# Optimization experiments

Measured on AMD Instinct MI355X. Metric: run time of the kernel, lower is better.

Reference implementation:

```python
import jax, jax.numpy as jnp
import numpy as np

N_NODES = 50000
N_EDGES = 1600000
IN_CH = 128
HEADS = 4
OUT_PER_HEAD = 32  # out_channels // heads with concat=True
NEG_SLOPE = 0.2    # GATConv default leaky_relu slope
SOFTMAX_EPS = 1e-16  # PyG scatter-softmax denominator eps
LN_EPS = 1e-5


def setup_inputs() -> dict:
    key = jax.random.key(0)
    ks = jax.random.split(key, 8)
    x = jax.random.normal(ks[0], (N_NODES, IN_CH), dtype=jnp.float32)
    edge_index = jax.random.randint(ks[1], (2, N_EDGES), 0, N_NODES, dtype=jnp.int32)
    W = jax.random.normal(ks[2], (IN_CH, HEADS * OUT_PER_HEAD), dtype=jnp.float32) * (1.0 / np.sqrt(IN_CH))
    att_src = jax.random.normal(ks[3], (HEADS, OUT_PER_HEAD), dtype=jnp.float32) * 0.1
    att_dst = jax.random.normal(ks[4], (HEADS, OUT_PER_HEAD), dtype=jnp.float32) * 0.1
    bias = jnp.zeros((HEADS * OUT_PER_HEAD,), dtype=jnp.float32)
    gamma = jnp.ones((HEADS * OUT_PER_HEAD,), dtype=jnp.float32)
    beta = jnp.zeros((HEADS * OUT_PER_HEAD,), dtype=jnp.float32)
    return {"x": x, "edge_index": edge_index, "W": W, "att_src": att_src,
            "att_dst": att_dst, "bias": bias, "gamma": gamma, "beta": beta}


def reference(x, edge_index, W, att_src, att_dst, bias, gamma, beta):
    N = x.shape[0]
    H, C = att_src.shape
    # GATConv default add_self_loops=True
    loop = jnp.arange(N, dtype=edge_index.dtype)
    src = jnp.concatenate([edge_index[0], loop])  # message source j
    dst = jnp.concatenate([edge_index[1], loop])  # aggregation target i

    h = (x @ W).reshape(N, H, C)                      # [N,H,C]
    a_s = jnp.einsum('nhc,hc->nh', h, att_src)        # [N,H]
    a_d = jnp.einsum('nhc,hc->nh', h, att_dst)        # [N,H]

    logits = jax.nn.leaky_relu(a_s[src] + a_d[dst], NEG_SLOPE)  # [E,H]
    # segment softmax over edges grouped by destination node
    m = jax.ops.segment_max(logits, dst, num_segments=N)        # [N,H]
    m = jnp.where(jnp.isfinite(m), m, 0.0)
    e = jnp.exp(logits - m[dst])
    s = jax.ops.segment_sum(e, dst, num_segments=N)             # [N,H]
    alpha = e / (s[dst] + SOFTMAX_EPS)                          # [E,H]

    msg = h[src] * alpha[:, :, None]                            # [E,H,C]
    out = jax.ops.segment_sum(msg, dst, num_segments=N)         # [N,H,C]
    out = out.reshape(N, H * C) + bias

    mu = out.mean(axis=-1, keepdims=True)
    var = ((out - mu) ** 2).mean(axis=-1, keepdims=True)
    y = (out - mu) / jnp.sqrt(var + LN_EPS) * gamma + beta
    return jax.nn.elu(y)
```

## Files before the change

### kernel.cpp

```cpp
#include <hip/hip_runtime.h>
#include <hip/hip_bf16.h>

typedef __hip_bfloat16 bf16;
typedef unsigned int u32;
typedef unsigned short u16;

constexpr int N   = 50000;
constexpr int E   = 1600000;
constexpr int C   = 128;
constexpr int H   = 4;
constexpr int NB  = 782;
constexpr int CAP = 2560;
constexpr int CHUNK = 4096;
constexpr float NEG  = 0.2f;
constexpr float SEPS = 1e-16f;
constexpr float LEPS = 1e-5f;

__device__ __forceinline__ float lo16(u32 v) { return __uint_as_float(v << 16); }
__device__ __forceinline__ float hi16(u32 v) { return __uint_as_float(v & 0xFFFF0000u); }

__global__ __launch_bounds__(256) void k1_gemm(
    const float* __restrict__ x, const float* __restrict__ W,
    const float* __restrict__ att_s, const float* __restrict__ att_d,
    bf16* __restrict__ hb, float* __restrict__ as_, float* __restrict__ ad_)
{
    const int nb = blockIdx.x * 16;
    const int t  = threadIdx.x;
    __shared__ float sx[16 * 128];
    const float4* xg = (const float4*)(x + nb * 128);
    ((float4*)sx)[t]       = xg[t];
    ((float4*)sx)[t + 256] = xg[t + 256];
    __syncthreads();

    const int c = t & 127;
    const int g = t >> 7;
    const float* xb = sx + (g << 10);
    float acc[8] = {0.f, 0.f, 0.f, 0.f, 0.f, 0.f, 0.f, 0.f};

    for (int k = 0; k < 128; k += 4) {
        const float w0 = W[(k + 0) * 128 + c];
        const float w1 = W[(k + 1) * 128 + c];
        const float w2 = W[(k + 2) * 128 + c];
        const float w3 = W[(k + 3) * 128 + c];
#pragma unroll
        for (int j = 0; j < 8; ++j) {
            const float4 xv = *(const float4*)(xb + j * 128 + k);
            acc[j] = fmaf(xv.x, w0, fmaf(xv.y, w1, fmaf(xv.z, w2, fmaf(xv.w, w3, acc[j]))));
        }
    }

    const int lane = t & 63;
    const int head = c >> 5;
    const float asc = att_s[c], adc = att_d[c];
#pragma unroll
    for (int j = 0; j < 8; ++j) {
        const int node = nb + (g << 3) + j;
        hb[node * 128 + c] = __float2bfloat16(acc[j]);
        float vs = acc[j] * asc;
        float vd = acc[j] * adc;
#pragma unroll
        for (int off = 16; off; off >>= 1) {
            vs += __shfl_xor(vs, off, 64);
            vd += __shfl_xor(vd, off, 64);
        }
        if ((lane & 31) == 0) {
            as_[node * H + head] = vs;
            ad_[node * H + head] = vd;
        }
    }
}

__global__ __launch_bounds__(256) void kbin(
    const int* __restrict__ ei, u32* __restrict__ gcur, u32* __restrict__ pairs)
{
    __shared__ u32 lcnt[NB], lbase[NB], lfill[NB];
    const int t = threadIdx.x;
    const int base = blockIdx.x * CHUNK;
    const int nE = min(CHUNK, E - base);
    for (int i = t; i < NB; i += 256) lcnt[i] = 0;
    __syncthreads();
    for (int i = t; i < nE; i += 256)
        atomicAdd(&lcnt[((u32)ei[E + base + i]) >> 6], 1u);
    __syncthreads();
    for (int i = t; i < NB; i += 256) {
        u32 cb = lcnt[i];
        lbase[i] = cb ? atomicAdd(&gcur[i], cb) : 0u;
        lfill[i] = 0u;
    }
    __syncthreads();
    for (int i = t; i < nE; i += 256) {
        u32 src = (u32)ei[base + i];
        u32 dst = (u32)ei[E + base + i];
        u32 b = dst >> 6;
        u32 pos = atomicAdd(&lfill[b], 1u);
        pairs[(size_t)b * CAP + lbase[b] + pos] = src | ((dst & 63u) << 16);
    }
}

__global__ __launch_bounds__(64) void kscan(
    const u32* __restrict__ gcur, u32* __restrict__ bbase, int* __restrict__ row_ptr)
{
    const int t = threadIdx.x;
    u32 vals[13];
    u32 s = 0;
#pragma unroll
    for (int i = 0; i < 13; ++i) {
        int idx = t * 13 + i;
        u32 v = (idx < NB) ? gcur[idx] : 0u;
        vals[i] = s; s += v;
    }
    u32 incl = s;
#pragma unroll
    for (int off = 1; off < 64; off <<= 1) {
        u32 u = __shfl_up(incl, off, 64);
        if (t >= off) incl += u;
    }
    const u32 excl = incl - s;
#pragma unroll
    for (int i = 0; i < 13; ++i) {
        int idx = t * 13 + i;
        if (idx < NB) bbase[idx] = excl + vals[i];
    }
    if (t == 0) row_ptr[N] = E;
}

__global__ __launch_bounds__(256) void kfill2(
    const u32* __restrict__ pairs, const u32* __restrict__ gcur,
    const u32* __restrict__ bbase, int* __restrict__ row_ptr, u16* __restrict__ col)
{
    __shared__ int jcnt[64], joff[64], jcur[64];
    const int b = blockIdx.x, t = threadIdx.x;
    const int cntb = (int)gcur[b];
    const int base = (int)bbase[b];
    if (t < 64) jcnt[t] = 0;
    __syncthreads();
    const u32* pr = pairs + (size_t)b * CAP;
    for (int i = t; i < cntb; i += 256) atomicAdd(&jcnt[pr[i] >> 16], 1);
    __syncthreads();
    if (t < 64) {
        int v = jcnt[t], incl = v;
#pragma unroll
        for (int off = 1; off < 64; off <<= 1) {
            int u = __shfl_up(incl, off, 64);
            if (t >= off) incl += u;
        }
        joff[t] = incl - v;
        const int n = b * 64 + t;
        if (n < N) row_ptr[n] = base + joff[t];
        jcur[t] = 0;
    }
    __syncthreads();
    for (int i = t; i < cntb; i += 256) {
        const u32 p = pr[i];
        const int j = p >> 16;
        const int pos = atomicAdd(&jcur[j], 1);
        col[base + joff[j] + pos] = (u16)(p & 0xFFFFu);
    }
}

__global__ __launch_bounds__(256) void kd_agg_ln(
    const int* __restrict__ row_ptr, const u16* __restrict__ col,
    const u32* __restrict__ hb, const float* __restrict__ as_,
    const float* __restrict__ ad_,
    const float* __restrict__ bias, const float* __restrict__ gamma,
    const float* __restrict__ beta, float* __restrict__ out)
{
    __shared__ float wlds[4][64];
    const int tid  = threadIdx.x;
    const int lane = tid & 63;
    const int wv   = __builtin_amdgcn_readfirstlane(tid >> 6);
    const int n    = __builtin_amdgcn_readfirstlane((int)blockIdx.x * 4 + (tid >> 6));
    if (n >= N) return;

    const int head  = lane >> 4;
    const int eoff  = lane & 15;
    const int wbase = head << 4;
    float* __restrict__ wrow = wlds[wv];

    const float adn = ad_[n * H + head];
    const float asn = as_[n * H + head];

    float ls = asn + adn;
    ls = fmaxf(ls, NEG * ls);
    const float wself = __expf(ls);
    float den = (eoff == 0) ? wself : 0.f;
    const u32 hvs = hb[n * 64 + lane];
    float num0 = wself * lo16(hvs);
    float num1 = wself * hi16(hvs);

    const int k0  = row_ptr[n];
    const int end = row_ptr[n + 1];

    for (int k = k0; k < end; k += 16) {
        const int cnt = min(16, end - k);
        int   colv = 0;
        float w    = 0.f;
        if (eoff < cnt) {
            colv = col[k + eoff];
            const float a = as_[colv * H + head];
            float le = a + adn;
            le = fmaxf(le, NEG * le);
            w = __expf(le);
        }
        den += w;
        wrow[lane] = w;

        int e = 0;
        for (; e + 4 <= cnt; e += 4) {
            const float4 w4 = *(const float4*)(wrow + wbase + e);
            const int s0 = __builtin_amdgcn_readlane(colv, e + 0);
            const int s1 = __builtin_amdgcn_readlane(colv, e + 1);
            const int s2 = __builtin_amdgcn_readlane(colv, e + 2);
            const int s3 = __builtin_amdgcn_readlane(colv, e + 3);
            const u32 v0 = hb[s0 * 64 + lane];
            const u32 v1 = hb[s1 * 64 + lane];
            const u32 v2 = hb[s2 * 64 + lane];
            const u32 v3 = hb[s3 * 64 + lane];
            num0 = fmaf(w4.x, lo16(v0), num0); num1 = fmaf(w4.x, hi16(v0), num1);
            num0 = fmaf(w4.y, lo16(v1), num0); num1 = fmaf(w4.y, hi16(v1), num1);
            num0 = fmaf(w4.z, lo16(v2), num0); num1 = fmaf(w4.z, hi16(v2), num1);
            num0 = fmaf(w4.w, lo16(v3), num0); num1 = fmaf(w4.w, hi16(v3), num1);
        }
        for (; e < cnt; ++e) {
            const float we = wrow[wbase + e];
            const int  s  = __builtin_amdgcn_readlane(colv, e);
            const u32  v  = hb[s * 64 + lane];
            num0 = fmaf(we, lo16(v), num0);
            num1 = fmaf(we, hi16(v), num1);
        }
    }

#pragma unroll
    for (int off = 1; off < 16; off <<= 1) den += __shfl_xor(den, off, 64);

    const int c0 = lane * 2;
    const float inv_den = 1.f / (den + SEPS);
    const float2 bi = *(const float2*)(bias + c0);
    float v0 = num0 * inv_den + bi.x;
    float v1 = num1 * inv_den + bi.y;

    float sum = v0 + v1;
#pragma unroll
    for (int off = 32; off; off >>= 1) sum += __shfl_xor(sum, off, 64);
    const float mu = sum * (1.0f / C);
    const float d0 = v0 - mu, d1 = v1 - mu;
    float sq = d0 * d0 + d1 * d1;
#pragma unroll
    for (int off = 32; off; off >>= 1) sq += __shfl_xor(sq, off, 64);
    const float inv = rsqrtf(sq * (1.0f / C) + LEPS);
    const float2 ga = *(const float2*)(gamma + c0);
    const float2 be = *(const float2*)(beta  + c0);
    float y0 = d0 * inv * ga.x + be.x;
    float y1 = d1 * inv * ga.y + be.y;
    y0 = y0 > 0.f ? y0 : __expf(y0) - 1.f;
    y1 = y1 > 0.f ? y1 : __expf(y1) - 1.f;
    float2 o; o.x = y0; o.y = y1;
    *(float2*)(out + (size_t)n * C + c0) = o;
}

extern "C" void kernel_launch(void* const* d_in, const int* in_sizes, int n_in,
                              void* d_out, int out_size, void* d_ws, size_t ws_size,
                              hipStream_t stream)
{
    const float* x     = (const float*)d_in[0];
    const int*   ei    = (const int*)  d_in[1];
    const float* W     = (const float*)d_in[2];
    const float* att_s = (const float*)d_in[3];
    const float* att_d = (const float*)d_in[4];
    const float* bias  = (const float*)d_in[5];
    const float* gamma = (const float*)d_in[6];
    const float* beta  = (const float*)d_in[7];
    float* out = (float*)d_out;

    char* p = (char*)d_ws;
    bf16*  hb      = (bf16*)p;   p += (size_t)N * C * sizeof(bf16);
    float* as_     = (float*)p;  p += (size_t)N * H * sizeof(float);
    float* ad_     = (float*)p;  p += (size_t)N * H * sizeof(float);
    u32*   pairs   = (u32*)p;    p += (size_t)NB * CAP * sizeof(u32);
    u16*   col     = (u16*)p;    p += ((size_t)E * sizeof(u16) + 15) & ~(size_t)15;
    int*   row_ptr = (int*)p;    p += ((size_t)(N + 1) * sizeof(int) + 15) & ~(size_t)15;
    u32*   gcur    = (u32*)p;    p += (size_t)NB * sizeof(u32);
    u32*   bbase   = (u32*)p;

    hipMemsetAsync(gcur, 0, NB * sizeof(u32), stream);
    k1_gemm<<<N / 16, 256, 0, stream>>>(x, W, att_s, att_d, hb, as_, ad_);
    kbin<<<(E + CHUNK - 1) / CHUNK, 256, 0, stream>>>(ei, gcur, pairs);
    kscan<<<1, 64, 0, stream>>>(gcur, bbase, row_ptr);
    kfill2<<<NB, 256, 0, stream>>>(pairs, gcur, bbase, row_ptr, col);
    kd_agg_ln<<<(N * 64) / 256, 256, 0, stream>>>(
        row_ptr, col, (const u32*)hb, as_, ad_, bias, gamma, beta, out);
}
```

Measured before the change: 239.8 us.

## Software-pipeline neighbor index and score loads, issue all 16 gathers per tile

The aggregation loop now prefetches column indices two tiles ahead and attention scores one tile ahead, so the index→score→exp dependency chain overlaps with the current tile's feature gathers. Each 16-edge tile issues all 16 row gathers unconditionally before the FMAs, with scheduling barriers to keep the loads grouped. Padding tiles use index 0 with zero weight, so they do redundant loads. The col buffer is padded so the prefetch may read past the end. This raises register pressure and wastes gathers on low-degree tail tiles.

```diff
diff --git a/kernel.cpp b/kernel.cpp
--- a/kernel.cpp
+++ b/kernel.cpp
@@ -189,45 +189,66 @@
     float num1 = wself * hi16(hvs);
 
     const int k0  = row_ptr[n];
-    const int end = row_ptr[n + 1];
-
-    for (int k = k0; k < end; k += 16) {
-        const int cnt = min(16, end - k);
-        int   colv = 0;
-        float w    = 0.f;
-        if (eoff < cnt) {
-            colv = col[k + eoff];
-            const float a = as_[colv * H + head];
-            float le = a + adn;
-            le = fmaxf(le, NEG * le);
-            w = __expf(le);
-        }
+    const int deg = row_ptr[n + 1] - k0;
+    const int ntiles = (deg + 15) >> 4;
+
+    const int cnt0 = deg < 16 ? deg : 16;
+    const int cnt1 = (deg - 16) < 16 ? (deg - 16) : 16;
+    int colv_cur = (eoff < cnt0) ? (int)col[k0 + eoff]      : 0;
+    int colv_nxt = (eoff < cnt1) ? (int)col[k0 + 16 + eoff] : 0;
+    float a_cur  = as_[colv_cur * H + head];
+    int cntc = cnt0, cntn = cnt1;
+
+    int k = k0;
+    for (int t = 0; t < ntiles; ++t, k += 16) {
+        const int rem2 = deg - 16 * (t + 2);
+        const int cnt2 = rem2 < 16 ? rem2 : 16;
+        const int cf_raw = (int)col[k + 32 + eoff];
+        const int colv_f = (eoff < cnt2) ? cf_raw : 0;
+
+        float le = a_cur + adn;
+        le = fmaxf(le, NEG * le);
+        const float w = (eoff < cntc) ? __expf(le) : 0.f;
         den += w;
         wrow[lane] = w;
-
-        int e = 0;
-        for (; e + 4 <= cnt; e += 4) {
-            const float4 w4 = *(const float4*)(wrow + wbase + e);
-            const int s0 = __builtin_amdgcn_readlane(colv, e + 0);
-            const int s1 = __builtin_amdgcn_readlane(colv, e + 1);
-            const int s2 = __builtin_amdgcn_readlane(colv, e + 2);
-            const int s3 = __builtin_amdgcn_readlane(colv, e + 3);
-            const u32 v0 = hb[s0 * 64 + lane];
-            const u32 v1 = hb[s1 * 64 + lane];
-            const u32 v2 = hb[s2 * 64 + lane];
-            const u32 v3 = hb[s3 * 64 + lane];
-            num0 = fmaf(w4.x, lo16(v0), num0); num1 = fmaf(w4.x, hi16(v0), num1);
-            num0 = fmaf(w4.y, lo16(v1), num0); num1 = fmaf(w4.y, hi16(v1), num1);
-            num0 = fmaf(w4.z, lo16(v2), num0); num1 = fmaf(w4.z, hi16(v2), num1);
-            num0 = fmaf(w4.w, lo16(v3), num0); num1 = fmaf(w4.w, hi16(v3), num1);
-        }
-        for (; e < cnt; ++e) {
-            const float we = wrow[wbase + e];
-            const int  s  = __builtin_amdgcn_readlane(colv, e);
-            const u32  v  = hb[s * 64 + lane];
-            num0 = fmaf(we, lo16(v), num0);
-            num1 = fmaf(we, hi16(v), num1);
-        }
+        const int colc = colv_cur;
+
+#define GL(i) const u32* rp##i = hb + ((size_t)(u32)__builtin_amdgcn_readlane(colc, i) << 6); \
+              const u32 v##i = rp##i[lane];
+        GL(0) GL(1) GL(2) GL(3) GL(4) GL(5) GL(6) GL(7)
+        GL(8) GL(9) GL(10) GL(11) GL(12) GL(13) GL(14) GL(15)
+#undef GL
+        __builtin_amdgcn_sched_barrier(0);
+
+        const float a_n = as_[colv_nxt * H + head];
+        __builtin_amdgcn_sched_barrier(0);
+
+        {
+            const float4 wa = *(const float4*)(wrow + wbase + 0);
+            num0 = fmaf(wa.x, lo16(v0), num0);  num1 = fmaf(wa.x, hi16(v0), num1);
+            num0 = fmaf(wa.y, lo16(v1), num0);  num1 = fmaf(wa.y, hi16(v1), num1);
+            num0 = fmaf(wa.z, lo16(v2), num0);  num1 = fmaf(wa.z, hi16(v2), num1);
+            num0 = fmaf(wa.w, lo16(v3), num0);  num1 = fmaf(wa.w, hi16(v3), num1);
+            const float4 wb = *(const float4*)(wrow + wbase + 4);
+            num0 = fmaf(wb.x, lo16(v4), num0);  num1 = fmaf(wb.x, hi16(v4), num1);
+            num0 = fmaf(wb.y, lo16(v5), num0);  num1 = fmaf(wb.y, hi16(v5), num1);
+            num0 = fmaf(wb.z, lo16(v6), num0);  num1 = fmaf(wb.z, hi16(v6), num1);
+            num0 = fmaf(wb.w, lo16(v7), num0);  num1 = fmaf(wb.w, hi16(v7), num1);
+            const float4 wc = *(const float4*)(wrow + wbase + 8);
+            num0 = fmaf(wc.x, lo16(v8), num0);  num1 = fmaf(wc.x, hi16(v8), num1);
+            num0 = fmaf(wc.y, lo16(v9), num0);  num1 = fmaf(wc.y, hi16(v9), num1);
+            num0 = fmaf(wc.z, lo16(v10), num0); num1 = fmaf(wc.z, hi16(v10), num1);
+            num0 = fmaf(wc.w, lo16(v11), num0); num1 = fmaf(wc.w, hi16(v11), num1);
+            const float4 wd = *(const float4*)(wrow + wbase + 12);
+            num0 = fmaf(wd.x, lo16(v12), num0); num1 = fmaf(wd.x, hi16(v12), num1);
+            num0 = fmaf(wd.y, lo16(v13), num0); num1 = fmaf(wd.y, hi16(v13), num1);
+            num0 = fmaf(wd.z, lo16(v14), num0); num1 = fmaf(wd.z, hi16(v14), num1);
+            num0 = fmaf(wd.w, lo16(v15), num0); num1 = fmaf(wd.w, hi16(v15), num1);
+        }
+
+        colv_cur = colv_nxt; colv_nxt = colv_f;
+        a_cur = a_n;
+        cntc = cntn; cntn = cnt2;
     }
 
 #pragma unroll
@@ -277,7 +298,7 @@
     float* as_     = (float*)p;  p += (size_t)N * H * sizeof(float);
     float* ad_     = (float*)p;  p += (size_t)N * H * sizeof(float);
     u32*   pairs   = (u32*)p;    p += (size_t)NB * CAP * sizeof(u32);
-    u16*   col     = (u16*)p;    p += ((size_t)E * sizeof(u16) + 15) & ~(size_t)15;
+    u16*   col     = (u16*)p;    p += ((size_t)(E + 64) * sizeof(u16) + 15) & ~(size_t)15;
     int*   row_ptr = (int*)p;    p += ((size_t)(N + 1) * sizeof(int) + 15) & ~(size_t)15;
     u32*   gcur    = (u32*)p;    p += (size_t)NB * sizeof(u32);
     u32*   bbase   = (u32*)p;
```

New measurement: 231.7 us. 1.03x faster.
